# Optimization experiments

Measured on AMD Instinct MI355X. Metric: run time of the kernel, lower is better.

The kernel has to match this reference:

```python
import jax, jax.numpy as jnp
import numpy as np

# Fixed-point fake quantization: 8 total bits, 4 fractional bits (STE for grads)
FRAC_BITS = 4
TOTAL_BITS = 8
SCALE = 2.0 ** FRAC_BITS
QMIN = float(-(2 ** (TOTAL_BITS - 1)))
QMAX = float(2 ** (TOTAL_BITS - 1) - 1)


def fake_quant(x):
    q = jnp.clip(jnp.round(x * SCALE), QMIN, QMAX) / SCALE
    # straight-through estimator
    return x + jax.lax.stop_gradient(q - x)


def setup_inputs() -> dict:
    key = jax.random.key(0)
    ks = jax.random.split(key, 5)
    S, B, I, H = 2048, 64, 128, 256
    std = 1.0 / np.sqrt(H)  # pytorch LSTMCell default init range
    return {
        "x": jax.random.normal(ks[0], (S, B, I), jnp.float32),
        "weight_ih": jax.random.uniform(ks[1], (4 * H, I), jnp.float32, -std, std),
        "weight_hh": jax.random.uniform(ks[2], (4 * H, H), jnp.float32, -std, std),
        "bias_ih": jax.random.uniform(ks[3], (4 * H,), jnp.float32, -std, std),
        "bias_hh": jax.random.uniform(ks[4], (4 * H,), jnp.float32, -std, std),
    }


def reference(x, weight_ih, weight_hh, bias_ih, bias_hh):
    # x: [S, B, I] (batch_first=False). Gate order i, f, g, o (pytorch LSTMCell).
    B = x.shape[1]
    H = weight_hh.shape[1]
    # weight quantization is state-independent -> hoist out of the scan
    wi = fake_quant(weight_ih)  # [4H, I]
    wh = fake_quant(weight_hh)  # [4H, H]
    bi = fake_quant(bias_ih)
    bh = fake_quant(bias_hh)

    def step(carry, x_t):
        h, c = carry
        hq = fake_quant(h)
        cq = fake_quant(c)
        gates = x_t @ wi.T + bi + hq @ wh.T + bh  # [B, 4H]
        i_g, f_g, g_g, o_g = jnp.split(gates, 4, axis=1)
        i = jax.nn.sigmoid(i_g)
        f = jax.nn.sigmoid(f_g)
        g = jnp.tanh(g_g)
        o = jax.nn.sigmoid(o_g)
        c1 = f * cq + i * g
        h1 = o * jnp.tanh(c1)
        return (h1, c1), h1

    zeros = jnp.zeros((B, H), x.dtype)
    (h_n, c_n), outputs = jax.lax.scan(step, (zeros, zeros), x)
    return outputs, h_n, c_n
```

## Files before the change

### kernel.cpp

```cpp
#include <hip/hip_runtime.h>
#include <math.h>

#define S_LEN 2048
#define BATCH 64
#define IN_D  128
#define HID   256
#define G4    1024

#if defined(__has_builtin)
# if __has_builtin(__builtin_amdgcn_sdot4)
#  define USE_SDOT4 1
# endif
#endif

__device__ __forceinline__ int dot4i8(int a, int b, int c) {
#ifdef USE_SDOT4
    return __builtin_amdgcn_sdot4(a, b, c, false);
#else
    int r = c;
    r += ((a << 24) >> 24) * ((b << 24) >> 24);
    r += ((a << 16) >> 24) * ((b << 16) >> 24);
    r += ((a <<  8) >> 24) * ((b <<  8) >> 24);
    r += ( a        >> 24) * ( b        >> 24);
    return r;
#endif
}

__device__ __forceinline__ float fq4(float x) {
    return fminf(fmaxf(rintf(x * 16.0f), -128.0f), 127.0f) * 0.0625f;
}

__device__ __forceinline__ float exp_vsl(float x) {
    const float xc = fminf(fmaxf(x, -88.3762626647949f), 88.3762626647950f);
    const float fx = floorf(fmaf(xc, 1.44269504088896341f, 0.5f));
    float r = fmaf(-fx, 0.693359375f, xc);
    r = fmaf(fx, 2.12194440e-4f, r);
    const float z = __fmul_rn(r, r);
    float y = fmaf(r, 1.9875691500e-4f, 1.3981999507e-3f);
    y = fmaf(y, r, 8.3334519073e-3f);
    y = fmaf(y, r, 4.1665795894e-2f);
    y = fmaf(y, r, 1.6666665459e-1f);
    y = fmaf(y, r, 5.0000001201e-1f);
    y = fmaf(y, z, r);
    y = __fadd_rn(y, 1.0f);
    const int n = (int)fx;
    const float sc = __int_as_float((n + 127) << 23);
    return __fmul_rn(y, sc);
}

__device__ __forceinline__ float tanh_vsl(float x) {
    const float xc = fminf(fmaxf(x, -9.0f), 9.0f);
    const float x2 = __fmul_rn(xc, xc);
    float p = -2.76076847742355e-16f;
    p = fmaf(p, x2, 2.00018790482477e-13f);
    p = fmaf(p, x2, -8.60467152213735e-11f);
    p = fmaf(p, x2, 5.12229709037114e-08f);
    p = fmaf(p, x2, 1.48572235717979e-05f);
    p = fmaf(p, x2, 6.37261928875436e-04f);
    p = fmaf(p, x2, 4.89352455891786e-03f);
    p = __fmul_rn(p, xc);
    float q = 1.19825839466702e-06f;
    q = fmaf(q, x2, 1.18534705686654e-04f);
    q = fmaf(q, x2, 2.26843463243900e-03f);
    q = fmaf(q, x2, 4.89352518554385e-03f);
    return __fdiv_rn(p, q);
}

__device__ __forceinline__ float sig_vsl(float x) {
    const float ef = exp_vsl(-x);
    return __fdiv_rn(1.0f, __fadd_rn(1.0f, ef));
}

__global__ void qlstm_prep(const float* __restrict__ wih, const float* __restrict__ whh,
                           const float* __restrict__ bih, const float* __restrict__ bhh,
                           float* __restrict__ wiq, int* __restrict__ whq4,
                           float* __restrict__ biq, float* __restrict__ bhq,
                           float* __restrict__ c_state, int* __restrict__ hq_state) {
    const int idx = blockIdx.x * 256 + threadIdx.x;
    if (idx < G4 * IN_D) wiq[idx] = fq4(wih[idx]);
    if (idx < (HID / 4) * G4) {
        const int d = idx >> 10;
        const int j = idx & 1023;
        int pack = 0;
#pragma unroll
        for (int c = 0; c < 4; ++c) {
            const int k = d * 4 + c;
            float q = fminf(fmaxf(rintf(whh[j * HID + k] * 16.0f), -128.0f), 127.0f);
            int qi = (int)q;
            pack |= (qi & 0xff) << (8 * c);
        }
        whq4[(d >> 2) * 4096 + j * 4 + (d & 3)] = pack;
    }
    if (idx < G4) { biq[idx] = fq4(bih[idx]); bhq[idx] = fq4(bhh[idx]); }
    if (idx < BATCH * HID) c_state[idx] = 0.0f;
    if (idx < BATCH * (HID / 4)) hq_state[idx] = 0;
}

#define GPAD 132
__global__ __launch_bounds__(256, 1) void qlstm_gx(
    const float* __restrict__ X, const float* __restrict__ Wq,
    const float* __restrict__ biq, float* __restrict__ Gx, int Mc) {
    __shared__ float Xs[IN_D][GPAD];
    __shared__ float Ws[IN_D][GPAD];
    const int t  = threadIdx.x;
    const int m0 = blockIdx.x * 128;
    const int n0 = blockIdx.y * 128;

#pragma unroll
    for (int i = 0; i < 16; ++i) {
        const int flat = i * 256 + t;
        const int m  = flat >> 5;
        const int k4 = flat & 31;
        float4 v = make_float4(0.f, 0.f, 0.f, 0.f);
        if (m0 + m < Mc) v = *(const float4*)(X + (size_t)(m0 + m) * IN_D + k4 * 4);
        Xs[k4 * 4 + 0][m] = v.x; Xs[k4 * 4 + 1][m] = v.y;
        Xs[k4 * 4 + 2][m] = v.z; Xs[k4 * 4 + 3][m] = v.w;
        float4 w = *(const float4*)(Wq + (size_t)(n0 + m) * IN_D + k4 * 4);
        Ws[k4 * 4 + 0][m] = w.x; Ws[k4 * 4 + 1][m] = w.y;
        Ws[k4 * 4 + 2][m] = w.z; Ws[k4 * 4 + 3][m] = w.w;
    }
    __syncthreads();

    const int tx = t & 15, ty = t >> 4;
    float acc[8][8];
#pragma unroll
    for (int i = 0; i < 8; ++i)
#pragma unroll
        for (int j = 0; j < 8; ++j) acc[i][j] = 0.0f;

#pragma unroll 4
    for (int k = 0; k < IN_D; ++k) {
        float4 a0 = *(const float4*)&Xs[k][ty * 8];
        float4 a1 = *(const float4*)&Xs[k][ty * 8 + 4];
        float4 b0 = *(const float4*)&Ws[k][tx * 8];
        float4 b1 = *(const float4*)&Ws[k][tx * 8 + 4];
        const float a[8]  = {a0.x, a0.y, a0.z, a0.w, a1.x, a1.y, a1.z, a1.w};
        const float bb[8] = {b0.x, b0.y, b0.z, b0.w, b1.x, b1.y, b1.z, b1.w};
#pragma unroll
        for (int i = 0; i < 8; ++i)
#pragma unroll
            for (int j = 0; j < 8; ++j)
                acc[i][j] = __fadd_rn(acc[i][j], __fmul_rn(a[i], bb[j]));
    }

    float4 bv0 = *(const float4*)(biq + n0 + tx * 8);
    float4 bv1 = *(const float4*)(biq + n0 + tx * 8 + 4);
    const float bb[8] = {bv0.x, bv0.y, bv0.z, bv0.w, bv1.x, bv1.y, bv1.z, bv1.w};
#pragma unroll
    for (int i = 0; i < 8; ++i) {
        const int m = m0 + ty * 8 + i;
        if (m < Mc) {
            float o[8];
#pragma unroll
            for (int j = 0; j < 8; ++j) o[j] = __fadd_rn(acc[i][j], bb[j]);
            *(float4*)(Gx + (size_t)m * G4 + n0 + tx * 8)     = make_float4(o[0], o[1], o[2], o[3]);
            *(float4*)(Gx + (size_t)m * G4 + n0 + tx * 8 + 4) = make_float4(o[4], o[5], o[6], o[7]);
        }
    }
}

__global__ __launch_bounds__(1024) void qlstm_fused(
    const float* __restrict__ Gx_rd, float* __restrict__ Gx_wr,
    const float* __restrict__ Xn, const float* __restrict__ Wq,
    const float* __restrict__ biq, int Mc_next,
    const int* __restrict__ whq4, const float* __restrict__ bhq,
    float* __restrict__ out, float* __restrict__ c_state, int* __restrict__ hq_state,
    float* __restrict__ hn, float* __restrict__ cn, int s0, int CHc) {
    const int t = threadIdx.x;

    __shared__ float Xs[IN_D][GPAD];
    __shared__ float Ws[IN_D][GPAD];
    __shared__ __align__(16) int hq[2][64];
    __shared__ float gl[G4];

    if (blockIdx.x < 64) {
        const int b = blockIdx.x;

        const float bh = bhq[t];
        float creg = 0.0f;
        if (t < HID) creg = c_state[b * HID + t];
        if (t < 64)  hq[0][t] = hq_state[b * 64 + t];
        __syncthreads();

        float gx = Gx_rd[(size_t)b * G4 + t];

        for (int sl = 0; sl < CHc; ++sl) {
            const int p = sl & 1;
            float nx = 0.0f;
            if (sl + 1 < CHc) nx = Gx_rd[(size_t)((sl + 1) * BATCH + b) * G4 + t];

            const int4* __restrict__ wq = (const int4*)whq4;
            const int4* __restrict__ hv4 = (const int4*)hq[p];
            int ca0 = 0, ca1 = 0, ca2 = 0, ca3 = 0;
#pragma unroll
            for (int j = 0; j < 4; ++j) {
                const int4 wv = wq[j * 1024 + t];
                const int4 hv = hv4[j];
                ca0 = dot4i8(wv.x, hv.x, ca0);
                ca0 = dot4i8(wv.y, hv.y, ca0);
                ca0 = dot4i8(wv.z, hv.z, ca0);
                ca0 = dot4i8(wv.w, hv.w, ca0);
            }
#pragma unroll
            for (int j = 4; j < 8; ++j) {
                const int4 wv = wq[j * 1024 + t];
                const int4 hv = hv4[j];
                ca1 = dot4i8(wv.x, hv.x, ca1);
                ca1 = dot4i8(wv.y, hv.y, ca1);
                ca1 = dot4i8(wv.z, hv.z, ca1);
                ca1 = dot4i8(wv.w, hv.w, ca1);
            }
#pragma unroll
            for (int j = 8; j < 12; ++j) {
                const int4 wv = wq[j * 1024 + t];
                const int4 hv = hv4[j];
                ca2 = dot4i8(wv.x, hv.x, ca2);
                ca2 = dot4i8(wv.y, hv.y, ca2);
                ca2 = dot4i8(wv.z, hv.z, ca2);
                ca2 = dot4i8(wv.w, hv.w, ca2);
            }
#pragma unroll
            for (int j = 12; j < 16; ++j) {
                const int4 wv = wq[j * 1024 + t];
                const int4 hv = hv4[j];
                ca3 = dot4i8(wv.x, hv.x, ca3);
                ca3 = dot4i8(wv.y, hv.y, ca3);
                ca3 = dot4i8(wv.z, hv.z, ca3);
                ca3 = dot4i8(wv.w, hv.w, ca3);
            }
            const int acc = (ca0 + ca1) + (ca2 + ca3);

            const float hh = (float)acc * 0.00390625f;
            const float gate = __fadd_rn(__fadd_rn(gx, hh), bh);

            float tv;
            if (t < 512)       tv = sig_vsl(gate);
            else if (t < 768)  tv = tanh_vsl(gate);
            else               tv = sig_vsl(gate);
            gl[t] = tv;
            __syncthreads();

            if (t < HID) {
                const float fv = gl[t + 256];
                const float gv = gl[t + 512];
                const float ov = gl[t + 768];
                const float cq = fminf(fmaxf(rintf(__fmul_rn(creg, 16.0f)), -128.0f), 127.0f) * 0.0625f;
                const float c1 = fmaf(fv, cq, __fmul_rn(tv, gv));
                const float h1 = __fmul_rn(ov, tanh_vsl(c1));
                creg = c1;
                out[(size_t)((s0 + sl) * BATCH + b) * HID + t] = h1;
                const int hb = (int)fminf(fmaxf(rintf(__fmul_rn(h1, 16.0f)), -128.0f), 127.0f);
                ((signed char*)hq[p ^ 1])[t] = (signed char)hb;
                if (s0 + sl == S_LEN - 1) {
                    hn[b * HID + t] = h1;
                    cn[b * HID + t] = c1;
                }
            }
            __syncthreads();
            gx = nx;
        }

        if (t < 64)  hq_state[b * 64 + t] = hq[CHc & 1][t];
        if (t < HID) c_state[b * HID + t] = creg;
    } else if (Mc_next > 0) {
        const int wid = blockIdx.x - 64;
        const int tiles_m = (Mc_next + 127) / 128;
        const int total = tiles_m * 8;
        const int tx = t & 31, ty = t >> 5;

        for (int tile = wid; tile < total; tile += 192) {
            const int m0 = (tile >> 3) * 128;
            const int n0 = (tile & 7) * 128;

#pragma unroll
            for (int i = 0; i < 4; ++i) {
                const int flat = i * 1024 + t;
                const int m  = flat >> 5;
                const int k4 = flat & 31;
                float4 v = make_float4(0.f, 0.f, 0.f, 0.f);
                if (m0 + m < Mc_next) v = *(const float4*)(Xn + (size_t)(m0 + m) * IN_D + k4 * 4);
                Xs[k4 * 4 + 0][m] = v.x; Xs[k4 * 4 + 1][m] = v.y;
                Xs[k4 * 4 + 2][m] = v.z; Xs[k4 * 4 + 3][m] = v.w;
                float4 w = *(const float4*)(Wq + (size_t)(n0 + m) * IN_D + k4 * 4);
                Ws[k4 * 4 + 0][m] = w.x; Ws[k4 * 4 + 1][m] = w.y;
                Ws[k4 * 4 + 2][m] = w.z; Ws[k4 * 4 + 3][m] = w.w;
            }
            __syncthreads();

            float acc[4][4];
#pragma unroll
            for (int i = 0; i < 4; ++i)
#pragma unroll
                for (int j = 0; j < 4; ++j) acc[i][j] = 0.0f;

#pragma unroll 4
            for (int k = 0; k < IN_D; ++k) {
                float4 av = *(const float4*)&Xs[k][ty * 4];
                float4 bv = *(const float4*)&Ws[k][tx * 4];
                const float a[4]  = {av.x, av.y, av.z, av.w};
                const float bb[4] = {bv.x, bv.y, bv.z, bv.w};
#pragma unroll
                for (int i = 0; i < 4; ++i)
#pragma unroll
                    for (int j = 0; j < 4; ++j)
                        acc[i][j] = __fadd_rn(acc[i][j], __fmul_rn(a[i], bb[j]));
            }

            float4 bv = *(const float4*)(biq + n0 + tx * 4);
            const float bb[4] = {bv.x, bv.y, bv.z, bv.w};
#pragma unroll
            for (int i = 0; i < 4; ++i) {
                const int m = m0 + ty * 4 + i;
                if (m < Mc_next) {
                    float o[4];
#pragma unroll
                    for (int j = 0; j < 4; ++j) o[j] = __fadd_rn(acc[i][j], bb[j]);
                    *(float4*)(Gx_wr + (size_t)m * G4 + n0 + tx * 4) = make_float4(o[0], o[1], o[2], o[3]);
                }
            }
            __syncthreads();
        }
    }
}

extern "C" void kernel_launch(void* const* d_in, const int* in_sizes, int n_in,
                              void* d_out, int out_size, void* d_ws, size_t ws_size,
                              hipStream_t stream) {
    (void)in_sizes; (void)n_in; (void)out_size;
    const float* x   = (const float*)d_in[0];
    const float* wih = (const float*)d_in[1];
    const float* whh = (const float*)d_in[2];
    const float* bih = (const float*)d_in[3];
    const float* bhh = (const float*)d_in[4];

    float* out = (float*)d_out;
    float* hn  = out + (size_t)S_LEN * BATCH * HID;
    float* cn  = hn + (size_t)BATCH * HID;

    char* ws = (char*)d_ws;
    const size_t off_wiq  = 0;
    const size_t off_biq  = off_wiq  + 524288;
    const size_t off_bhq  = off_biq  + 4096;
    const size_t off_c    = off_bhq  + 4096;
    const size_t off_hq   = off_c    + 65536;
    const size_t off_whq4 = off_hq   + 16384;
    const size_t off_gx   = off_whq4 + 262144;

    float* wiq     = (float*)(ws + off_wiq);
    float* biq     = (float*)(ws + off_biq);
    float* bhq     = (float*)(ws + off_bhq);
    float* c_state = (float*)(ws + off_c);
    int*   hq_st   = (int*)  (ws + off_hq);
    int*   whq4    = (int*)  (ws + off_whq4);
    float* gxbase  = (float*)(ws + off_gx);

    const size_t per_step = (size_t)BATCH * G4 * 4;
    size_t avail = (ws_size > off_gx) ? (ws_size - off_gx) : 0;
    int CH = (int)(avail / (2 * per_step));
    if (CH > 512) CH = 512;
    if (CH < 1) CH = 1;
    float* gxb[2] = { gxbase, gxbase + (size_t)CH * BATCH * G4 };

    qlstm_prep<<<512, 256, 0, stream>>>(wih, whh, bih, bhh, wiq, whq4, biq, bhq, c_state, hq_st);

    const int CHc0 = (S_LEN < CH) ? S_LEN : CH;
    const int Mc0  = CHc0 * BATCH;
    {
        dim3 grid((Mc0 + 127) / 128, G4 / 128);
        qlstm_gx<<<grid, 256, 0, stream>>>(x, wiq, biq, gxb[0], Mc0);
    }

    int k = 0;
    for (int s0 = 0; s0 < S_LEN; s0 += CH, ++k) {
        const int CHc = (S_LEN - s0 < CH) ? (S_LEN - s0) : CH;
        const int ns0 = s0 + CHc;
        const int Mc_next = (ns0 < S_LEN) ? (((S_LEN - ns0 < CH) ? (S_LEN - ns0) : CH) * BATCH) : 0;
        qlstm_fused<<<256, 1024, 0, stream>>>(
            gxb[k & 1], gxb[(k + 1) & 1],
            x + (size_t)ns0 * BATCH * IN_D, wiq, biq, Mc_next,
            whq4, bhq, out, c_state, hq_st, hn, cn, s0, CHc);
    }
}
```

Before: 2.688 ms.

## Keep quantized recurrent weights in registers with 512-thread fused blocks

The recurrent blocks drop from 1024 to 512 threads, and each thread now handles two gate rows. Each thread's int8 recurrent weights (two rows × 64 ints) are loaded once into registers rather than re-read from global or cache on every timestep. Shared memory is unioned between the recurrence and GEMM paths, the f/o gates are exchanged as float2 instead of a full gate array, and the GEMM tile gives each thread 8x4 outputs. The chunk size cap is halved and GPAD changes to 129. The risks are register pressure from the 128-int weight arrays, possible spills, and GPAD 129 breaking float4 alignment in the LDS reads.

```diff
diff --git a/kernel.cpp b/kernel.cpp
--- a/kernel.cpp
+++ b/kernel.cpp
@@ -96,7 +96,7 @@
     if (idx < BATCH * (HID / 4)) hq_state[idx] = 0;
 }
 
-#define GPAD 132
+#define GPAD 129
 __global__ __launch_bounds__(256, 1) void qlstm_gx(
     const float* __restrict__ X, const float* __restrict__ Wq,
     const float* __restrict__ biq, float* __restrict__ Gx, int Mc) {
@@ -159,7 +159,8 @@
     }
 }
 
-__global__ __launch_bounds__(1024) void qlstm_fused(
+__attribute__((amdgpu_waves_per_eu(2)))
+__global__ __launch_bounds__(512) void qlstm_fused(
     const float* __restrict__ Gx_rd, float* __restrict__ Gx_wr,
     const float* __restrict__ Xn, const float* __restrict__ Wq,
     const float* __restrict__ biq, int Mc_next,
@@ -167,102 +168,118 @@
     float* __restrict__ out, float* __restrict__ c_state, int* __restrict__ hq_state,
     float* __restrict__ hn, float* __restrict__ cn, int s0, int CHc) {
     const int t = threadIdx.x;
-
-    __shared__ float Xs[IN_D][GPAD];
-    __shared__ float Ws[IN_D][GPAD];
-    __shared__ __align__(16) int hq[2][64];
-    __shared__ float gl[G4];
+    __shared__ __align__(16) char smem[2 * IN_D * GPAD * 4];
 
     if (blockIdx.x < 64) {
         const int b = blockIdx.x;
-
-        const float bh = bhq[t];
+        int*    hqb = (int*)smem;
+        float2* fo  = (float2*)(smem + 512);
+
+        const int4* __restrict__ wq4 = (const int4*)whq4;
+        int4 wlo[16], whi[16];
+#pragma unroll
+        for (int j = 0; j < 16; ++j) {
+            wlo[j] = wq4[j * 1024 + t];
+            whi[j] = wq4[j * 1024 + t + 512];
+        }
+
+        const float bh0 = bhq[t];
+        const float bh1 = bhq[t + 512];
+
         float creg = 0.0f;
         if (t < HID) creg = c_state[b * HID + t];
-        if (t < 64)  hq[0][t] = hq_state[b * 64 + t];
+        if (t < 64)  hqb[t] = hq_state[b * 64 + t];
         __syncthreads();
 
-        float gx = Gx_rd[(size_t)b * G4 + t];
+        float gx0 = Gx_rd[(size_t)b * G4 + t];
+        float gx1 = Gx_rd[(size_t)b * G4 + t + 512];
 
         for (int sl = 0; sl < CHc; ++sl) {
             const int p = sl & 1;
-            float nx = 0.0f;
-            if (sl + 1 < CHc) nx = Gx_rd[(size_t)((sl + 1) * BATCH + b) * G4 + t];
-
-            const int4* __restrict__ wq = (const int4*)whq4;
-            const int4* __restrict__ hv4 = (const int4*)hq[p];
+            float nx0 = 0.0f, nx1 = 0.0f;
+            if (sl + 1 < CHc) {
+                const size_t base = (size_t)((sl + 1) * BATCH + b) * G4;
+                nx0 = Gx_rd[base + t];
+                nx1 = Gx_rd[base + t + 512];
+            }
+
+            const int4* __restrict__ hv4 = (const int4*)(hqb + p * 64);
             int ca0 = 0, ca1 = 0, ca2 = 0, ca3 = 0;
+            int cb0 = 0, cb1 = 0, cb2 = 0, cb3 = 0;
 #pragma unroll
             for (int j = 0; j < 4; ++j) {
-                const int4 wv = wq[j * 1024 + t];
                 const int4 hv = hv4[j];
-                ca0 = dot4i8(wv.x, hv.x, ca0);
-                ca0 = dot4i8(wv.y, hv.y, ca0);
-                ca0 = dot4i8(wv.z, hv.z, ca0);
-                ca0 = dot4i8(wv.w, hv.w, ca0);
+                ca0 = dot4i8(wlo[j].x, hv.x, ca0); ca0 = dot4i8(wlo[j].y, hv.y, ca0);
+                ca0 = dot4i8(wlo[j].z, hv.z, ca0); ca0 = dot4i8(wlo[j].w, hv.w, ca0);
+                cb0 = dot4i8(whi[j].x, hv.x, cb0); cb0 = dot4i8(whi[j].y, hv.y, cb0);
+                cb0 = dot4i8(whi[j].z, hv.z, cb0); cb0 = dot4i8(whi[j].w, hv.w, cb0);
             }
 #pragma unroll
             for (int j = 4; j < 8; ++j) {
-                const int4 wv = wq[j * 1024 + t];
                 const int4 hv = hv4[j];
-                ca1 = dot4i8(wv.x, hv.x, ca1);
-                ca1 = dot4i8(wv.y, hv.y, ca1);
-                ca1 = dot4i8(wv.z, hv.z, ca1);
-                ca1 = dot4i8(wv.w, hv.w, ca1);
+                ca1 = dot4i8(wlo[j].x, hv.x, ca1); ca1 = dot4i8(wlo[j].y, hv.y, ca1);
+                ca1 = dot4i8(wlo[j].z, hv.z, ca1); ca1 = dot4i8(wlo[j].w, hv.w, ca1);
+                cb1 = dot4i8(whi[j].x, hv.x, cb1); cb1 = dot4i8(whi[j].y, hv.y, cb1);
+                cb1 = dot4i8(whi[j].z, hv.z, cb1); cb1 = dot4i8(whi[j].w, hv.w, cb1);
             }
 #pragma unroll
             for (int j = 8; j < 12; ++j) {
-                const int4 wv = wq[j * 1024 + t];
                 const int4 hv = hv4[j];
-                ca2 = dot4i8(wv.x, hv.x, ca2);
-                ca2 = dot4i8(wv.y, hv.y, ca2);
-                ca2 = dot4i8(wv.z, hv.z, ca2);
-                ca2 = dot4i8(wv.w, hv.w, ca2);
+                ca2 = dot4i8(wlo[j].x, hv.x, ca2); ca2 = dot4i8(wlo[j].y, hv.y, ca2);
+                ca2 = dot4i8(wlo[j].z, hv.z, ca2); ca2 = dot4i8(wlo[j].w, hv.w, ca2);
+                cb2 = dot4i8(whi[j].x, hv.x, cb2); cb2 = dot4i8(whi[j].y, hv.y, cb2);
+                cb2 = dot4i8(whi[j].z, hv.z, cb2); cb2 = dot4i8(whi[j].w, hv.w, cb2);
             }
 #pragma unroll
             for (int j = 12; j < 16; ++j) {
-                const int4 wv = wq[j * 1024 + t];
                 const int4 hv = hv4[j];
-                ca3 = dot4i8(wv.x, hv.x, ca3);
-                ca3 = dot4i8(wv.y, hv.y, ca3);
-                ca3 = dot4i8(wv.z, hv.z, ca3);
-                ca3 = dot4i8(wv.w, hv.w, ca3);
-            }
-            const int acc = (ca0 + ca1) + (ca2 + ca3);
-
-            const float hh = (float)acc * 0.00390625f;
-            const float gate = __fadd_rn(__fadd_rn(gx, hh), bh);
-
-            float tv;
-            if (t < 512)       tv = sig_vsl(gate);
-            else if (t < 768)  tv = tanh_vsl(gate);
-            else               tv = sig_vsl(gate);
-            gl[t] = tv;
+                ca3 = dot4i8(wlo[j].x, hv.x, ca3); ca3 = dot4i8(wlo[j].y, hv.y, ca3);
+                ca3 = dot4i8(wlo[j].z, hv.z, ca3); ca3 = dot4i8(wlo[j].w, hv.w, ca3);
+                cb3 = dot4i8(whi[j].x, hv.x, cb3); cb3 = dot4i8(whi[j].y, hv.y, cb3);
+                cb3 = dot4i8(whi[j].z, hv.z, cb3); cb3 = dot4i8(whi[j].w, hv.w, cb3);
+            }
+            const int accl = (ca0 + ca1) + (ca2 + ca3);
+            const int acch = (cb0 + cb1) + (cb2 + cb3);
+
+            const float hh0 = (float)accl * 0.00390625f;
+            const float hh1 = (float)acch * 0.00390625f;
+            const float gate0 = __fadd_rn(__fadd_rn(gx0, hh0), bh0);
+            const float gate1 = __fadd_rn(__fadd_rn(gx1, hh1), bh1);
+
+            float tv0, tv1;
+            if (t < HID) {
+                tv0 = sig_vsl(gate0);
+                tv1 = tanh_vsl(gate1);
+            } else {
+                tv0 = sig_vsl(gate0);
+                tv1 = sig_vsl(gate1);
+                fo[t - HID] = make_float2(tv0, tv1);
+            }
             __syncthreads();
 
             if (t < HID) {
-                const float fv = gl[t + 256];
-                const float gv = gl[t + 512];
-                const float ov = gl[t + 768];
+                const float2 f_o = fo[t];
                 const float cq = fminf(fmaxf(rintf(__fmul_rn(creg, 16.0f)), -128.0f), 127.0f) * 0.0625f;
-                const float c1 = fmaf(fv, cq, __fmul_rn(tv, gv));
-                const float h1 = __fmul_rn(ov, tanh_vsl(c1));
+                const float c1 = fmaf(f_o.x, cq, __fmul_rn(tv0, tv1));
+                const float h1 = __fmul_rn(f_o.y, tanh_vsl(c1));
                 creg = c1;
                 out[(size_t)((s0 + sl) * BATCH + b) * HID + t] = h1;
                 const int hb = (int)fminf(fmaxf(rintf(__fmul_rn(h1, 16.0f)), -128.0f), 127.0f);
-                ((signed char*)hq[p ^ 1])[t] = (signed char)hb;
+                ((signed char*)(hqb + (p ^ 1) * 64))[t] = (signed char)hb;
                 if (s0 + sl == S_LEN - 1) {
                     hn[b * HID + t] = h1;
                     cn[b * HID + t] = c1;
                 }
             }
             __syncthreads();
-            gx = nx;
+            gx0 = nx0; gx1 = nx1;
         }
 
-        if (t < 64)  hq_state[b * 64 + t] = hq[CHc & 1][t];
+        if (t < 64)  hq_state[b * 64 + t] = hqb[(CHc & 1) * 64 + t];
         if (t < HID) c_state[b * HID + t] = creg;
     } else if (Mc_next > 0) {
+        float (*Xs)[GPAD] = (float(*)[GPAD])smem;
+        float (*Ws)[GPAD] = (float(*)[GPAD])(smem + IN_D * GPAD * 4);
         const int wid = blockIdx.x - 64;
         const int tiles_m = (Mc_next + 127) / 128;
         const int total = tiles_m * 8;
@@ -273,8 +290,8 @@
             const int n0 = (tile & 7) * 128;
 
 #pragma unroll
-            for (int i = 0; i < 4; ++i) {
-                const int flat = i * 1024 + t;
+            for (int i = 0; i < 8; ++i) {
+                const int flat = i * 512 + t;
                 const int m  = flat >> 5;
                 const int k4 = flat & 31;
                 float4 v = make_float4(0.f, 0.f, 0.f, 0.f);
@@ -287,20 +304,21 @@
             }
             __syncthreads();
 
-            float acc[4][4];
-#pragma unroll
-            for (int i = 0; i < 4; ++i)
+            float acc[8][4];
+#pragma unroll
+            for (int i = 0; i < 8; ++i)
 #pragma unroll
                 for (int j = 0; j < 4; ++j) acc[i][j] = 0.0f;
 
 #pragma unroll 4
             for (int k = 0; k < IN_D; ++k) {
-                float4 av = *(const float4*)&Xs[k][ty * 4];
+                float4 a0 = *(const float4*)&Xs[k][ty * 8];
+                float4 a1 = *(const float4*)&Xs[k][ty * 8 + 4];
                 float4 bv = *(const float4*)&Ws[k][tx * 4];
-                const float a[4]  = {av.x, av.y, av.z, av.w};
+                const float a[8]  = {a0.x, a0.y, a0.z, a0.w, a1.x, a1.y, a1.z, a1.w};
                 const float bb[4] = {bv.x, bv.y, bv.z, bv.w};
 #pragma unroll
-                for (int i = 0; i < 4; ++i)
+                for (int i = 0; i < 8; ++i)
 #pragma unroll
                     for (int j = 0; j < 4; ++j)
                         acc[i][j] = __fadd_rn(acc[i][j], __fmul_rn(a[i], bb[j]));
@@ -309,8 +327,8 @@
             float4 bv = *(const float4*)(biq + n0 + tx * 4);
             const float bb[4] = {bv.x, bv.y, bv.z, bv.w};
 #pragma unroll
-            for (int i = 0; i < 4; ++i) {
-                const int m = m0 + ty * 4 + i;
+            for (int i = 0; i < 8; ++i) {
+                const int m = m0 + ty * 8 + i;
                 if (m < Mc_next) {
                     float o[4];
 #pragma unroll
@@ -357,7 +375,7 @@
     const size_t per_step = (size_t)BATCH * G4 * 4;
     size_t avail = (ws_size > off_gx) ? (ws_size - off_gx) : 0;
     int CH = (int)(avail / (2 * per_step));
-    if (CH > 512) CH = 512;
+    if (CH > 256) CH = 256;
     if (CH < 1) CH = 1;
     float* gxb[2] = { gxbase, gxbase + (size_t)CH * BATCH * G4 };
 
@@ -375,7 +393,7 @@
         const int CHc = (S_LEN - s0 < CH) ? (S_LEN - s0) : CH;
         const int ns0 = s0 + CHc;
         const int Mc_next = (ns0 < S_LEN) ? (((S_LEN - ns0 < CH) ? (S_LEN - ns0) : CH) * BATCH) : 0;
-        qlstm_fused<<<256, 1024, 0, stream>>>(
+        qlstm_fused<<<256, 512, 0, stream>>>(
             gxb[k & 1], gxb[(k + 1) & 1],
             x + (size_t)ns0 * BATCH * IN_D, wiq, biq, Mc_next,
             whq4, bhq, out, c_state, hq_st, hn, cn, s0, CHc);
```

After: 3.341 ms. +24.3%, slower.
